# Optimization experiments

Hardware: AMD Instinct MI355X
Metric: run time of the kernel (lower is better)

Reference implementation:

```python
import jax, jax.numpy as jnp
import numpy as np

B, L, D, H, K = 1, 1024, 512, 8, 24
h = D // H
EPS = 1e-5


def setup_inputs() -> dict:
    key = jax.random.key(0)
    ks = jax.random.split(key, 8)
    s = 0.02
    return {
        "x": jax.random.normal(ks[0], (B, L, D), jnp.float32),
        "Wq": jax.random.normal(ks[1], (D, D), jnp.float32) * s,
        "bq": jnp.zeros((D,), jnp.float32),
        "Wk": jax.random.normal(ks[2], (D, D), jnp.float32) * s,
        "bk": jnp.zeros((D,), jnp.float32),
        "Wv": jax.random.normal(ks[3], (D, D), jnp.float32) * s,
        "bv": jnp.zeros((D,), jnp.float32),
        "Wo": jax.random.normal(ks[4], (D, D), jnp.float32) * s,
        "bo": jnp.zeros((D,), jnp.float32),
        "Wg": jax.random.normal(ks[5], (h * h, 1), jnp.float32) * s,
        "bg": jnp.zeros((1,), jnp.float32),
        "kv_norm_scale": jnp.ones((1, H, 1, h, h), jnp.float32),
        "qk_norm_scale": jnp.full((1, H, 1), 1.0 / np.sqrt(h), jnp.float32),
        "spectral_filters": jax.random.normal(ks[6], (L, K), jnp.float32) * 0.1,
    }


def _full_conv(filters, u, n_fft, L_out):
    # filters: [L, K], u: [B, H, L, h] -> causal FFT conv: [B, H, L, K, h]
    Ff = jnp.fft.rfft(filters, n=n_fft, axis=0)            # [F, K]
    U = jnp.fft.rfft(u, n=n_fft, axis=2)                    # [B, H, F, h]
    y = jnp.fft.irfft(U[:, :, :, None, :] * Ff[None, None, :, :, None], n=n_fft, axis=2)
    return y[:, :, :L_out]


def reference(x, Wq, bq, Wk, bk, Wv, bv, Wo, bo, Wg, bg,
              kv_norm_scale, qk_norm_scale, spectral_filters):
    Bb, Ll, Dd = x.shape
    q = (x @ Wq + bq).reshape(Bb, Ll, H, h).transpose(0, 2, 1, 3)  # [B,H,L,h]
    k = (x @ Wk + bk).reshape(Bb, Ll, H, h).transpose(0, 2, 1, 3)
    v = (x @ Wv + bv).reshape(Bb, Ll, H, h).transpose(0, 2, 1, 3)

    sim = jnp.einsum("bhld,bhld->bhl", q, k) * qk_norm_scale       # [B,H,L]

    # F.normalize(dim=-1)
    k = k / jnp.maximum(jnp.linalg.norm(k, axis=-1, keepdims=True), 1e-12)
    v = v / jnp.maximum(jnp.linalg.norm(v, axis=-1, keepdims=True), 1e-12)

    n_fft = 2 * Ll
    k = _full_conv(spectral_filters, k, n_fft, Ll)  # [B,H,L,K,h]
    v = _full_conv(spectral_filters, v, n_fft, Ll)

    Z = jnp.einsum("bhlkd,bhlke->bhlde", v, k) * kv_norm_scale     # [B,H,L,h,h]

    logits = Z.reshape(Bb, H, Ll, h * h) @ Wg + bg                  # [B,H,L,1]
    gates = jax.nn.relu(logits) ** 2 + EPS
    gates = gates[..., None]                                        # [B,H,L,1,1]
    gated_Z = gates * Z

    # Online-softmax associative scan over L for (m, s); Z/g combine is pure add -> cumsum.
    def combine(a, b):
        m_x, s_x = a
        m_y, s_y = b
        m = jnp.maximum(m_x, m_y)
        return (m, s_x * jnp.exp(m_x - m) + s_y * jnp.exp(m_y - m))

    m_scan, s_scan = jax.lax.associative_scan(combine, (sim, jnp.ones_like(sim)), axis=2)
    Z_scan = jnp.cumsum(gated_Z, axis=2)
    g_scan = jnp.cumsum(gates, axis=2)

    softmax_w = jnp.exp(sim - m_scan)[..., None, None] / (s_scan[..., None, None] + EPS)
    gated_w = Z_scan / (g_scan + EPS)
    attn = gated_w * (1.0 + jax.nn.silu(softmax_w))                 # [B,H,L,h,h]

    ctxt = jnp.einsum("bhld,bhlde->bhle", q, attn)                  # [B,H,L,h]
    ctxt = ctxt.transpose(0, 2, 1, 3).reshape(Bb, Ll, Dd)
    return ctxt @ Wo + bo
```

## Files before the change

### kernel.cpp

```cpp
#include <hip/hip_runtime.h>
#include <math.h>

#define Hh 8
#define Ll 1024
#define KF 24
#define Dm 512
#define EPSf 1e-5f
#define LK (Ll*KF)

typedef __attribute__((ext_vector_type(8))) short sh8;
typedef __attribute__((ext_vector_type(4))) short sh4;
typedef __attribute__((ext_vector_type(4))) float f32x4;

#define OFF_SIM    1572864
#define OFF_LOGITS 1581056
#define OFF_GATES  1589248
#define OFF_FACTOR 1597440
#define OFF_VCB    1605632
#define OFF_KCB    7897088
#define OFF_QPK    14188544
#define OFF_MPK    14450688
#define OFF_WOPK   14467072
#define OFF_CPK    14598144
#define OFF_CZP    26771456
#define OFF_S0     28868608
#define OFF_CPART  29392896
#define OFF_FPK_F  26771456
#define OFF_UPK_F  27607040
#define OFF_APK_F  28131328
#define OFF_BPK_F  28393472

__device__ inline unsigned short f2bf(float x){
    unsigned int u = __float_as_uint(x);
    unsigned int r = (u + 0x7fffu + ((u>>16)&1u)) >> 16;
    return (unsigned short)r;
}
__device__ inline float bf2f(unsigned short u){ return __uint_as_float(((unsigned int)u)<<16); }
__device__ inline sh8 ld8_8B(const unsigned short* p){
    union { sh8 s; sh4 h[2]; } u;
    u.h[0] = *(const sh4*)(p);
    u.h[1] = *(const sh4*)(p+4);
    return u.s;
}

__global__ __launch_bounds__(256) void pack_all_kernel(
    const float* __restrict__ x,
    const float* __restrict__ Wq, const float* __restrict__ Wk, const float* __restrict__ Wv,
    const float* __restrict__ Wo, const float* __restrict__ kvs, const float* __restrict__ Wg,
    const float* __restrict__ filt,
    unsigned short* __restrict__ Apk, unsigned short* __restrict__ Bpk,
    unsigned short* __restrict__ Wopk, unsigned short* __restrict__ Mpk,
    unsigned short* __restrict__ Fpk16, float* __restrict__ logits)
{
    int bid = blockIdx.x, tid = threadIdx.x;
    if (bid < 64){
        int mb = bid;
        for (int ks=0; ks<16; ks++){
            #pragma unroll
            for (int p=0;p<2;p++){
                int e = tid + p*256;
                int lane = e>>3, j = e&7;
                int m = mb*16 + (lane&15);
                int k = ks*32 + ((lane>>4)&3)*8 + j;
                Apk[(mb*16+ks)*512 + e] = f2bf(x[m*Dm + k]);
            }
        }
    } else if (bid < 160){
        int nb = bid - 64;
        int n0 = nb*16;
        int mm = n0>>9;
        const float* W = (mm==0)?Wq:((mm==1)?Wk:Wv);
        int coff = n0 & 511;
        for (int ks=0; ks<16; ks++){
            #pragma unroll
            for (int p=0;p<2;p++){
                int e = tid + p*256;
                int lane = e>>3, j = e&7;
                int kk = ks*32 + ((lane>>4)&3)*8 + j;
                Bpk[(nb*16+ks)*512 + e] = f2bf(W[kk*Dm + coff + (lane&15)]);
            }
        }
    } else if (bid < 192){
        int nb = bid - 160;
        int n0 = nb*16;
        for (int ks=0; ks<16; ks++){
            #pragma unroll
            for (int p=0;p<2;p++){
                int e = tid + p*256;
                int lane = e>>3, j = e&7;
                int kk = ks*32 + ((lane>>4)&3)*8 + j;
                Wopk[(nb*16+ks)*512 + e] = f2bf(Wo[kk*Dm + n0 + (lane&15)]);
            }
        }
    } else if (bid < 200){
        int hd = bid - 192;
        for (int it=0; it<16; it++){
            int idx = tid + it*256;
            int f = idx & 511, ksnb = idx >> 9;
            int nb = ksnb>>1, ks = ksnb&1;
            int lane = f>>3, j = f&7;
            int e = nb*16 + (lane&15);
            int d = ks*32 + ((lane>>4)&3)*8 + j;
            Mpk[hd*4096 + idx] = f2bf(kvs[(hd*64+e)*64 + d]*Wg[e*64+d]);
        }
    } else if (bid < 296){
        int b2 = bid - 200;
        for (int ti=0; ti<16; ti++){
            int tile = b2*16 + ti;
            int kf = tile>>6, d16 = tile&63;
            unsigned short* dst = Fpk16 + tile*1024;
            #pragma unroll
            for (int p2=0;p2<4;p2++){
                int e = tid + p2*256;
                int ks = e>>9, f = e&511;
                int lane = f>>3, j = f&7;
                int m = lane&15;
                int k = ks*32 + ((lane>>4)&3)*8 + j;
                int fidx = 16*d16 + m - k;
                float v = (fidx>=0 && fidx<Ll) ? filt[fidx*KF+kf] : 0.0f;
                dst[e] = f2bf(v);
            }
        }
    } else {
        for (int i=tid; i<Hh*Ll; i+=256) logits[i] = 0.f;
    }
}

__global__ __launch_bounds__(64) void qkvn_kernel(
    const unsigned short* __restrict__ Apk, const unsigned short* __restrict__ Bpk,
    const float* __restrict__ bq, const float* __restrict__ bk, const float* __restrict__ bv,
    const float* __restrict__ qks, float* __restrict__ simg,
    unsigned short* __restrict__ Upk, unsigned short* __restrict__ Qpk)
{
    int mb = blockIdx.x, hd = blockIdx.y;
    int lane = threadIdx.x, quad = lane>>4, lm = lane&15;
    f32x4 acc[3][4];
    #pragma unroll
    for (int mm=0;mm<3;mm++)
        #pragma unroll
        for (int nbl=0;nbl<4;nbl++) acc[mm][nbl]=(f32x4){0.f,0.f,0.f,0.f};
    for (int ks=0; ks<16; ks++){
        sh8 a = *(const sh8*)(Apk + (mb*16+ks)*512 + lane*8);
        #pragma unroll
        for (int mm=0;mm<3;mm++)
            #pragma unroll
            for (int nbl=0;nbl<4;nbl++){
                sh8 b = *(const sh8*)(Bpk + ((mm*32 + hd*4 + nbl)*16 + ks)*512 + lane*8);
                acc[mm][nbl] = __builtin_amdgcn_mfma_f32_16x16x32_bf16(a, b, acc[mm][nbl], 0,0,0);
            }
    }
    #pragma unroll
    for (int nbl=0;nbl<4;nbl++){
        float bqv = bq[hd*64 + nbl*16 + lm];
        float bkv = bk[hd*64 + nbl*16 + lm];
        float bvv = bv[hd*64 + nbl*16 + lm];
        #pragma unroll
        for (int r=0;r<4;r++){
            acc[0][nbl][r] += bqv; acc[1][nbl][r] += bkv; acc[2][nbl][r] += bvv;
        }
    }
    float simr[4], k2r[4], v2r[4];
    #pragma unroll
    for (int r=0;r<4;r++){
        float ps=0.f, pk=0.f, pv=0.f;
        #pragma unroll
        for (int nbl=0;nbl<4;nbl++){
            float qv=acc[0][nbl][r], kv=acc[1][nbl][r], vv=acc[2][nbl][r];
            ps += qv*kv; pk += kv*kv; pv += vv*vv;
        }
        #pragma unroll
        for (int off=1; off<16; off<<=1){
            ps += __shfl_xor(ps, off, 64);
            pk += __shfl_xor(pk, off, 64);
            pv += __shfl_xor(pv, off, 64);
        }
        simr[r]=ps; k2r[r]=pk; v2r[r]=pv;
    }
    float qksv = qks[hd];
    #pragma unroll
    for (int r=0;r<4;r++){
        int t = mb*16 + quad*4 + r;
        float invk = 1.f/fmaxf(sqrtf(k2r[r]), 1e-12f);
        float invv = 1.f/fmaxf(sqrtf(v2r[r]), 1e-12f);
        int ST = t>>6, ksb = (t>>5)&1, j = t&7;
        int rowf = ((t>>3)&3)*16 + lm;
        #pragma unroll
        for (int nbl=0;nbl<4;nbl++){
            int frag = ksb*2048 + nbl*512 + rowf*8 + j;
            Upk[((hd*16)+ST)*4096 + frag]     = f2bf(acc[2][nbl][r]*invv);
            Upk[(((8+hd)*16)+ST)*4096 + frag] = f2bf(acc[1][nbl][r]*invk);
            int d = nbl*16 + lm;
            int ks2 = d>>5, j2 = d&7, fl2 = ((d>>3)&3)*16 + (t&15);
            Qpk[((hd*64+mb)*2+ks2)*512 + fl2*8 + j2] = f2bf(acc[0][nbl][r]);
        }
        if (lm==0) simg[hd*Ll + t] = simr[r]*qksv;
    }
}

__device__ __forceinline__ void conv_phase(
    int T, int kf0, int hd,
    const unsigned short* __restrict__ Fpk16,
    const unsigned short* __restrict__ Uv, const unsigned short* __restrict__ Uk,
    const unsigned short* __restrict__ Mh,
    unsigned short* __restrict__ vcb, unsigned short* __restrict__ kcb,
    float* __restrict__ logits, unsigned short* lds,
    int tid, int w, int lane)
{
    int quad = lane>>4, lm = lane&15;
    f32x4 acc[3][2][4];
    #pragma unroll
    for (int kf=0;kf<3;kf++)
        #pragma unroll
        for (int tz=0;tz<2;tz++)
            #pragma unroll
            for (int nb=0;nb<4;nb++) acc[kf][tz][nb]=(f32x4){0.f,0.f,0.f,0.f};

    __syncthreads();
    {
        sh8 v0=*(const sh8*)(Uv+tid*8), v1=*(const sh8*)(Uv+(tid+256)*8);
        sh8 k0=*(const sh8*)(Uk+tid*8), k1=*(const sh8*)(Uk+(tid+256)*8);
        *(sh8*)(&lds[tid*8])=v0; *(sh8*)(&lds[(tid+256)*8])=v1;
        *(sh8*)(&lds[4096+tid*8])=k0; *(sh8*)(&lds[4096+(tid+256)*8])=k1;
    }
    for (int ST=0; ST<=T; ST++){
        sh8 nv0,nv1,nk0,nk1;
        bool more = (ST < T);
        if (more){
            const unsigned short* Uvn = Uv + (ST+1)*4096;
            const unsigned short* Ukn = Uk + (ST+1)*4096;
            nv0=*(const sh8*)(Uvn+tid*8); nv1=*(const sh8*)(Uvn+(tid+256)*8);
            nk0=*(const sh8*)(Ukn+tid*8); nk1=*(const sh8*)(Ukn+(tid+256)*8);
        }
        int d16 = 4*(T-ST) + w;
        sh8 a[3][2];
        #pragma unroll
        for (int kf=0;kf<3;kf++)
            #pragma unroll
            for (int ks=0;ks<2;ks++)
                a[kf][ks] = *(const sh8*)(Fpk16 + ((kf0+kf)*64 + d16)*1024 + ks*512 + lane*8);
        __syncthreads();
        const unsigned short* Bb = &lds[(ST&1)*8192];
        #pragma unroll
        for (int ks=0;ks<2;ks++)
            #pragma unroll
            for (int nb=0;nb<4;nb++){
                sh8 bv = *(const sh8*)(Bb + ks*2048 + nb*512 + lane*8);
                sh8 bk = *(const sh8*)(Bb + 4096 + ks*2048 + nb*512 + lane*8);
                #pragma unroll
                for (int kf=0;kf<3;kf++){
                    acc[kf][0][nb] = __builtin_amdgcn_mfma_f32_16x16x32_bf16(
                        a[kf][ks], bv, acc[kf][0][nb], 0,0,0);
                    acc[kf][1][nb] = __builtin_amdgcn_mfma_f32_16x16x32_bf16(
                        a[kf][ks], bk, acc[kf][1][nb], 0,0,0);
                }
            }
        if (more){
            unsigned short* Bn = &lds[((ST+1)&1)*8192];
            *(sh8*)(Bn+tid*8)=nv0; *(sh8*)(Bn+(tid+256)*8)=nv1;
            *(sh8*)(Bn+4096+tid*8)=nk0; *(sh8*)(Bn+4096+(tid+256)*8)=nk1;
        }
    }
    float logacc[4] = {0.f,0.f,0.f,0.f};
    #pragma unroll
    for (int kf=0;kf<3;kf++){
        __syncthreads();
        #pragma unroll
        for (int tz=0;tz<2;tz++)
            #pragma unroll
            for (int nb=0;nb<4;nb++)
                #pragma unroll
                for (int r=0;r<4;r++){
                    int tl = w*16 + quad*4 + r;
                    lds[tz*4608 + tl*72 + nb*16 + lm] = f2bf(acc[kf][tz][nb][r]);
                }
        __syncthreads();
        #pragma unroll
        for (int tz=0;tz<2;tz++){
            unsigned short* dst = tz ? kcb : vcb;
            #pragma unroll
            for (int it=0; it<2; it++){
                int idx = tid + it*256;
                int row = idx>>3, seg = idx&7;
                sh8 vv = *(const sh8*)(&lds[tz*4608 + row*72 + seg*8]);
                *(sh8*)(dst + ((hd*Ll + T*64 + row)*KF + kf0+kf)*64 + seg*8) = vv;
            }
        }
        f32x4 accp[4];
        #pragma unroll
        for (int nb=0;nb<4;nb++) accp[nb]=(f32x4){0.f,0.f,0.f,0.f};
        #pragma unroll
        for (int ks=0;ks<2;ks++){
            sh8 a2 = *(const sh8*)(&lds[4608 + (w*16+lm)*72 + ks*32 + quad*8]);
            #pragma unroll
            for (int nb=0;nb<4;nb++){
                sh8 bm = *(const sh8*)(Mh + (nb*2+ks)*512 + lane*8);
                accp[nb] = __builtin_amdgcn_mfma_f32_16x16x32_bf16(a2, bm, accp[nb], 0,0,0);
            }
        }
        #pragma unroll
        for (int r=0;r<4;r++){
            int rloc = w*16 + quad*4 + r;
            float s = 0.f;
            #pragma unroll
            for (int nb=0;nb<4;nb++)
                s += accp[nb][r]*bf2f(lds[rloc*72 + nb*16 + lm]);
            logacc[r] += s;
        }
    }
    #pragma unroll
    for (int r=0;r<4;r++){
        float s = logacc[r];
        s += __shfl_xor(s, 1, 64);
        s += __shfl_xor(s, 2, 64);
        s += __shfl_xor(s, 4, 64);
        s += __shfl_xor(s, 8, 64);
        if (lm==0)
            atomicAdd(&logits[hd*Ll + T*64 + w*16 + quad*4 + r], s);
    }
}

__global__ __launch_bounds__(256,2) void convf_kernel(
    const unsigned short* __restrict__ Fpk16, const unsigned short* __restrict__ Upk,
    const unsigned short* __restrict__ Mpk,
    unsigned short* __restrict__ vcb, unsigned short* __restrict__ kcb,
    float* __restrict__ logits)
{
    __shared__ unsigned short lds[16384];
    int p = blockIdx.x, kf0 = blockIdx.y*3, hd = blockIdx.z;
    int tid=threadIdx.x, w=tid>>6, lane=tid&63;
    const unsigned short* Uv = Upk + (hd*16)*4096;
    const unsigned short* Uk = Upk + ((8+hd)*16)*4096;
    const unsigned short* Mh = Mpk + hd*4096;
    conv_phase(15-p, kf0, hd, Fpk16, Uv, Uk, Mh, vcb, kcb, logits, lds, tid, w, lane);
    conv_phase(p,    kf0, hd, Fpk16, Uv, Uk, Mh, vcb, kcb, logits, lds, tid, w, lane);
}

__global__ __launch_bounds__(256) void scan_kernel(
    const float* __restrict__ simg, const float* __restrict__ logits,
    const float* __restrict__ bg, float* __restrict__ gates, float* __restrict__ factor)
{
    int hd=blockIdx.x, tid=threadIdx.x;
    __shared__ float sm[256], ssc[256], sg[256];
    float bgv = bg[0];
    float simv[4], m_loc[4], s_loc[4], g_loc[4];
    float m = -__builtin_inff(), s = 0.f, g = 0.f;
    for(int e=0;e<4;e++){
        int ix = hd*Ll + tid*4 + e;
        simv[e] = simg[ix];
        float lg = logits[ix] + bgv;
        float r = fmaxf(lg, 0.f);
        float gv = r*r + EPSf;
        gates[ix] = gv;
        float mn = fmaxf(m, simv[e]);
        s = s*__expf(m-mn) + __expf(simv[e]-mn);
        m = mn; g += gv;
        m_loc[e]=m; s_loc[e]=s; g_loc[e]=g;
    }
    sm[tid]=m; ssc[tid]=s; sg[tid]=g;
    __syncthreads();
    for(int off=1; off<256; off<<=1){
        float pm=0, ps=0, pg=0; bool has = (tid>=off);
        if(has){ pm=sm[tid-off]; ps=ssc[tid-off]; pg=sg[tid-off]; }
        __syncthreads();
        if(has){
            float mn=fmaxf(pm, sm[tid]);
            float sn=ps*__expf(pm-mn) + ssc[tid]*__expf(sm[tid]-mn);
            sm[tid]=mn; ssc[tid]=sn; sg[tid]=pg+sg[tid];
        }
        __syncthreads();
    }
    float pm=-__builtin_inff(), ps=0.f, pg=0.f;
    if (tid>0){ pm=sm[tid-1]; ps=ssc[tid-1]; pg=sg[tid-1]; }
    for(int e=0;e<4;e++){
        float mn=fmaxf(pm, m_loc[e]);
        float sn=ps*__expf(pm-mn) + s_loc[e]*__expf(m_loc[e]-mn);
        float gn=pg + g_loc[e];
        float sw = __expf(simv[e]-mn)/(sn+EPSf);
        float silu = sw/(1.f+__expf(-sw));
        factor[hd*Ll + tid*4 + e] = (1.f+silu)/(gn+EPSf);
    }
}

#define VTS 68
#define ASS 72
__global__ __launch_bounds__(256) void p3cz_kernel(
    const unsigned short* __restrict__ Qpk,
    const unsigned short* __restrict__ vcb, const unsigned short* __restrict__ kcb,
    const float* __restrict__ gates, float* __restrict__ cpart,
    unsigned short* __restrict__ czp)
{
    __shared__ unsigned short VT[64*VTS];
    __shared__ unsigned short KT[64*VTS];
    __shared__ unsigned short As[4][16*ASS];
    __shared__ unsigned short Vraw[64*72];
    __shared__ float gl[16];
    int tid=threadIdx.x, w=tid>>6, lane=tid&63;
    int quad=lane>>4, lm=lane&15;
    int c=blockIdx.x, qq=blockIdx.y, hd=blockIdx.z;
    int T0=c*64, tq0=T0+qq*16, RQ0=tq0*KF;
    if (tid<16) gl[tid]=gates[hd*Ll+tq0+tid];
    sh8 aq[2];
    {
        const unsigned short* qb = Qpk + ((hd*64 + (c*4+w))*2)*512;
        aq[0] = *(const sh8*)(qb + lane*8);
        aq[1] = *(const sh8*)(qb + 512 + lane*8);
    }
    f32x4 ctx[4], cz[4];
    #pragma unroll
    for (int nb=0;nb<4;nb++){ ctx[nb]=(f32x4){0,0,0,0}; cz[nb]=(f32x4){0,0,0,0}; }
    int t_g = T0 + w*16 + quad*4;
    int rp = tid>>3, e0 = (tid&7)*8, r0 = rp*2;

    sh8 pv0, pv1, pk0, pk1;
    {
        const unsigned short* vrow = vcb + (hd*LK + RQ0)*64;
        const unsigned short* krow = kcb + (hd*LK + RQ0)*64;
        pv0 = *(const sh8*)(vrow + r0*64 + e0);
        pv1 = *(const sh8*)(vrow + (r0+1)*64 + e0);
        pk0 = *(const sh8*)(krow + r0*64 + e0);
        pk1 = *(const sh8*)(krow + (r0+1)*64 + e0);
    }
    for (int sub=0; sub<6; sub++){
        int RB = RQ0 + sub*64;
        __syncthreads();
        {
            float g0 = gl[(RB + r0)/KF - tq0];
            float g1 = gl[(RB + r0 + 1)/KF - tq0];
            *(sh8*)(&Vraw[r0*72 + e0]) = pv0;
            *(sh8*)(&Vraw[(r0+1)*72 + e0]) = pv1;
            #pragma unroll
            for (int j=0;j<8;j++){
                unsigned int pv = (unsigned int)f2bf(bf2f((unsigned short)pv0[j])*g0)
                                | ((unsigned int)f2bf(bf2f((unsigned short)pv1[j])*g1)<<16);
                *(unsigned int*)(&VT[(e0+j)*VTS + r0]) = pv;
                unsigned int pk = (unsigned int)(unsigned short)pk0[j]
                                | ((unsigned int)(unsigned short)pk1[j]<<16);
                *(unsigned int*)(&KT[(e0+j)*VTS + r0]) = pk;
            }
        }
        if (sub < 5){
            const unsigned short* vrow = vcb + (hd*LK + RB + 64)*64;
            const unsigned short* krow = kcb + (hd*LK + RB + 64)*64;
            pv0 = *(const sh8*)(vrow + r0*64 + e0);
            pv1 = *(const sh8*)(vrow + (r0+1)*64 + e0);
            pk0 = *(const sh8*)(krow + r0*64 + e0);
            pk1 = *(const sh8*)(krow + (r0+1)*64 + e0);
        }
        __syncthreads();
        f32x4 S[4];
        #pragma unroll
        for (int nb=0;nb<4;nb++) S[nb]=(f32x4){0,0,0,0};
        #pragma unroll
        for (int ks=0;ks<2;ks++){
            #pragma unroll
            for (int nb=0;nb<4;nb++){
                sh8 b = *(const sh8*)(&Vraw[(nb*16+lm)*72 + ks*32 + quad*8]);
                S[nb] = __builtin_amdgcn_mfma_f32_16x16x32_bf16(aq[ks], b, S[nb], 0,0,0);
            }
        }
        #pragma unroll
        for (int nb=0;nb<4;nb++){
            int row_l = nb*16+lm;
            int tp = (RB + row_l)/KF;
            float g = gl[tp - tq0];
            #pragma unroll
            for (int r=0;r<4;r++){
                float v = (t_g + r >= tp) ? S[nb][r]*g : 0.f;
                As[w][(quad*4+r)*ASS + row_l] = f2bf(v);
            }
        }
        #pragma unroll
        for (int ks=0;ks<2;ks++){
            sh8 a2 = *(const sh8*)(&As[w][lm*ASS + ks*32 + quad*8]);
            sh8 av = ld8_8B(&VT[(w*16+lm)*VTS + ks*32 + quad*8]);
            #pragma unroll
            for (int nb=0;nb<4;nb++){
                sh8 bk = ld8_8B(&KT[(nb*16+lm)*VTS + ks*32 + quad*8]);
                ctx[nb] = __builtin_amdgcn_mfma_f32_16x16x32_bf16(a2, bk, ctx[nb], 0,0,0);
                cz[nb]  = __builtin_amdgcn_mfma_f32_16x16x32_bf16(av, bk, cz[nb], 0,0,0);
            }
        }
    }
    #pragma unroll
    for (int nb=0;nb<4;nb++){
        #pragma unroll
        for (int r=0;r<4;r++){
            cpart[((qq*8+hd)*Ll + t_g + r)*64 + nb*16+lm] = ctx[nb][r];
        }
    }
    int ob = ((hd*16+c)*4+qq)*4096;
    #pragma unroll
    for (int nb=0;nb<4;nb++){
        #pragma unroll
        for (int r=0;r<4;r++){
            czp[ob + (w*16+quad*4+r)*64 + nb*16+lm] = f2bf(cz[nb][r]);
        }
    }
}

__global__ __launch_bounds__(256) void s0_kernel(
    const unsigned short* __restrict__ czp, unsigned short* __restrict__ S0b)
{
    int idx = blockIdx.x*256 + threadIdx.x;
    int hd = blockIdx.y;
    int d = idx>>6, e = idx&63;
    int frag = (d>>5)*2048 + (e>>4)*512 + ((((d>>3)&3)*16) + (e&15))*8 + (d&7);
    float a = 0.f;
    for (int c=0;c<16;c++){
        S0b[(hd*16+c)*4096 + frag] = f2bf(a);
        int b = ((hd*16+c)*4)*4096 + idx;
        a += bf2f(czp[b]) + bf2f(czp[b+4096]) + bf2f(czp[b+2*4096]) + bf2f(czp[b+3*4096]);
    }
}

__global__ __launch_bounds__(256) void combine_kernel(
    const unsigned short* __restrict__ Qpk, const unsigned short* __restrict__ S0b,
    const float* __restrict__ cpart, const float* __restrict__ factor,
    unsigned short* __restrict__ Cpk)
{
    int c=blockIdx.x, hd=blockIdx.y;
    int tid=threadIdx.x, wid=tid>>6, lane=tid&63, quad=lane>>4, lm=lane&15;
    int mb = c*4 + wid;
    sh8 aq0 = *(const sh8*)(Qpk + ((hd*64+mb)*2)*512 + lane*8);
    sh8 aq1 = *(const sh8*)(Qpk + ((hd*64+mb)*2+1)*512 + lane*8);
    const unsigned short* sb = S0b + (hd*16+c)*4096;
    f32x4 acc[4];
    #pragma unroll
    for (int nb=0;nb<4;nb++) acc[nb]=(f32x4){0.f,0.f,0.f,0.f};
    #pragma unroll
    for (int ks=0;ks<2;ks++){
        sh8 a = ks ? aq1 : aq0;
        #pragma unroll
        for (int nb=0;nb<4;nb++){
            sh8 b = *(const sh8*)(sb + ks*2048 + nb*512 + lane*8);
            acc[nb] = __builtin_amdgcn_mfma_f32_16x16x32_bf16(a, b, acc[nb], 0,0,0);
        }
    }
    float fv[4];
    #pragma unroll
    for (int r=0;r<4;r++) fv[r] = factor[hd*Ll + mb*16 + quad*4 + r];
    #pragma unroll
    for (int nb=0;nb<4;nb++){
        int e = nb*16 + lm;
        int dim = hd*64 + e;
        int ks2 = dim>>5, koff = dim&31, qd = koff>>3, jj = koff&7;
        #pragma unroll
        for (int r=0;r<4;r++){
            int t = mb*16 + quad*4 + r;
            float v = acc[nb][r];
            #pragma unroll
            for (int q=0;q<4;q++) v += cpart[((q*8+hd)*Ll + t)*64 + e];
            v *= fv[r];
            Cpk[((t>>4)*16 + ks2)*512 + qd*128 + (t&15)*8 + jj] = f2bf(v);
        }
    }
}

__global__ __launch_bounds__(256) void outprojm_kernel(
    const unsigned short* __restrict__ Cpk, const unsigned short* __restrict__ Wopk,
    const float* __restrict__ bo, float* __restrict__ out)
{
    int mt=blockIdx.x, nt=blockIdx.y;
    int tid=threadIdx.x, wid=tid>>6, lane=tid&63;
    int mb=mt*4+wid;
    f32x4 acc[4];
    #pragma unroll
    for (int nb=0;nb<4;nb++) acc[nb]=(f32x4){0.f,0.f,0.f,0.f};
    for (int ks=0;ks<16;ks++){
        sh8 a = *(const sh8*)(Cpk + (mb*16+ks)*512 + lane*8);
        #pragma unroll
        for (int nb2=0;nb2<4;nb2++){
            sh8 b = *(const sh8*)(Wopk + ((nt*4+nb2)*16+ks)*512 + lane*8);
            acc[nb2] = __builtin_amdgcn_mfma_f32_16x16x32_bf16(a, b, acc[nb2], 0,0,0);
        }
    }
    int quad=lane>>4, col=lane&15;
    #pragma unroll
    for (int nb2=0;nb2<4;nb2++){
        int n = nt*64 + nb2*16 + col;
        float bval = bo[n];
        #pragma unroll
        for (int r=0;r<4;r++){
            out[(mb*16+quad*4+r)*Dm + n] = acc[nb2][r] + bval;
        }
    }
}

extern "C" void kernel_launch(void* const* d_in, const int* in_sizes, int n_in,
                              void* d_out, int out_size, void* d_ws, size_t ws_size,
                              hipStream_t stream)
{
    (void)in_sizes; (void)n_in; (void)out_size; (void)ws_size;
    const float* x   =(const float*)d_in[0];
    const float* Wq  =(const float*)d_in[1];
    const float* bq  =(const float*)d_in[2];
    const float* Wk  =(const float*)d_in[3];
    const float* bk  =(const float*)d_in[4];
    const float* Wv  =(const float*)d_in[5];
    const float* bv  =(const float*)d_in[6];
    const float* Wo  =(const float*)d_in[7];
    const float* bo  =(const float*)d_in[8];
    const float* Wg  =(const float*)d_in[9];
    const float* bg  =(const float*)d_in[10];
    const float* kvs =(const float*)d_in[11];
    const float* qks =(const float*)d_in[12];
    const float* filt=(const float*)d_in[13];
    float* ws = (float*)d_ws;
    float* simg  = ws+OFF_SIM;
    float* logits= ws+OFF_LOGITS;
    float* gates = ws+OFF_GATES;
    float* factor= ws+OFF_FACTOR;
    float* cpart = ws+OFF_CPART;
    unsigned short* vcb  = (unsigned short*)(ws + OFF_VCB);
    unsigned short* kcb  = (unsigned short*)(ws + OFF_KCB);
    unsigned short* Qpk  = (unsigned short*)(ws + OFF_QPK);
    unsigned short* Mpk  = (unsigned short*)(ws + OFF_MPK);
    unsigned short* Wopk = (unsigned short*)(ws + OFF_WOPK);
    unsigned short* Cpk  = (unsigned short*)(ws + OFF_CPK);
    unsigned short* czp  = (unsigned short*)(ws + OFF_CZP);
    unsigned short* S0b  = (unsigned short*)(ws + OFF_S0);
    unsigned short* Fpk16= (unsigned short*)(ws + OFF_FPK_F);
    unsigned short* Upk  = (unsigned short*)(ws + OFF_UPK_F);
    unsigned short* Apk  = (unsigned short*)(ws + OFF_APK_F);
    unsigned short* Bpk  = (unsigned short*)(ws + OFF_BPK_F);
    float* out   = (float*)d_out;

    pack_all_kernel<<<dim3(297),    256,0,stream>>>(x,Wq,Wk,Wv,Wo,kvs,Wg,filt,
                                                    Apk,Bpk,Wopk,Mpk,Fpk16,logits);
    qkvn_kernel   <<<dim3(64,8),    64, 0,stream>>>(Apk,Bpk,bq,bk,bv,qks,simg,Upk,Qpk);
    convf_kernel  <<<dim3(8,8,8),   256,0,stream>>>(Fpk16,Upk,Mpk,vcb,kcb,logits);
    scan_kernel   <<<dim3(8),       256,0,stream>>>(simg,logits,bg,gates,factor);
    p3cz_kernel   <<<dim3(16,4,8),  256,0,stream>>>(Qpk,vcb,kcb,gates,cpart,czp);
    s0_kernel     <<<dim3(16,8),    256,0,stream>>>(czp,S0b);
    combine_kernel<<<dim3(16,8),    256,0,stream>>>(Qpk,S0b,cpart,factor,Cpk);
    outprojm_kernel<<<dim3(16,8),   256,0,stream>>>(Cpk,Wopk,bo,out);
}
```

Baseline: 171.0 us.

## Fuse chunk-prefix sum into combine, atomically reduce cpart, stage filters in LDS

Removes the s0 kernel. Each combine block now computes its own exclusive prefix over earlier chunk partial sums of czp into shared memory. The four per-quarter ctx partials are now accumulated with float atomicAdd into one cpart buffer, which the pack kernel zeroes with 64 extra blocks, so combine reads one value instead of four. The filter-packing blocks also stage one filter column in LDS instead of doing strided global gathers. The trade-offs are redundant prefix work that grows with the chunk index, atomic contention, and sum order that is not deterministic.

```diff
diff --git a/kernel.cpp b/kernel.cpp
--- a/kernel.cpp
+++ b/kernel.cpp
@@ -23,7 +23,6 @@
 #define OFF_WOPK   14467072
 #define OFF_CPK    14598144
 #define OFF_CZP    26771456
-#define OFF_S0     28868608
 #define OFF_CPART  29392896
 #define OFF_FPK_F  26771456
 #define OFF_UPK_F  27607040
@@ -50,8 +49,10 @@
     const float* __restrict__ filt,
     unsigned short* __restrict__ Apk, unsigned short* __restrict__ Bpk,
     unsigned short* __restrict__ Wopk, unsigned short* __restrict__ Mpk,
-    unsigned short* __restrict__ Fpk16, float* __restrict__ logits)
-{
+    unsigned short* __restrict__ Fpk16, float* __restrict__ logits,
+    float* __restrict__ cpart)
+{
+    __shared__ float fl[1024];
     int bid = blockIdx.x, tid = threadIdx.x;
     if (bid < 64){
         int mb = bid;
@@ -105,10 +106,12 @@
         }
     } else if (bid < 296){
         int b2 = bid - 200;
+        int kf = b2>>2, g = b2&3;
+        for (int i=tid; i<1024; i+=256) fl[i] = filt[i*KF + kf];
+        __syncthreads();
         for (int ti=0; ti<16; ti++){
-            int tile = b2*16 + ti;
-            int kf = tile>>6, d16 = tile&63;
-            unsigned short* dst = Fpk16 + tile*1024;
+            int d16 = g*16 + ti;
+            unsigned short* dst = Fpk16 + (kf*64 + d16)*1024;
             #pragma unroll
             for (int p2=0;p2<4;p2++){
                 int e = tid + p2*256;
@@ -117,12 +120,16 @@
                 int m = lane&15;
                 int k = ks*32 + ((lane>>4)&3)*8 + j;
                 int fidx = 16*d16 + m - k;
-                float v = (fidx>=0 && fidx<Ll) ? filt[fidx*KF+kf] : 0.0f;
+                float v = (fidx>=0) ? fl[fidx] : 0.0f;
                 dst[e] = f2bf(v);
             }
         }
+    } else if (bid == 296){
+        for (int i=tid; i<Hh*Ll; i+=256) logits[i] = 0.f;
     } else {
-        for (int i=tid; i<Hh*Ll; i+=256) logits[i] = 0.f;
+        int zb = bid - 297;
+        int base = zb*8192;
+        for (int i=tid; i<8192; i+=256) cpart[base+i] = 0.f;
     }
 }
 
@@ -485,7 +492,7 @@
     for (int nb=0;nb<4;nb++){
         #pragma unroll
         for (int r=0;r<4;r++){
-            cpart[((qq*8+hd)*Ll + t_g + r)*64 + nb*16+lm] = ctx[nb][r];
+            atomicAdd(&cpart[(hd*Ll + t_g + r)*64 + nb*16+lm], ctx[nb][r]);
         }
     }
     int ob = ((hd*16+c)*4+qq)*4096;
@@ -498,32 +505,30 @@
     }
 }
 
-__global__ __launch_bounds__(256) void s0_kernel(
-    const unsigned short* __restrict__ czp, unsigned short* __restrict__ S0b)
-{
-    int idx = blockIdx.x*256 + threadIdx.x;
-    int hd = blockIdx.y;
-    int d = idx>>6, e = idx&63;
-    int frag = (d>>5)*2048 + (e>>4)*512 + ((((d>>3)&3)*16) + (e&15))*8 + (d&7);
-    float a = 0.f;
-    for (int c=0;c<16;c++){
-        S0b[(hd*16+c)*4096 + frag] = f2bf(a);
-        int b = ((hd*16+c)*4)*4096 + idx;
-        a += bf2f(czp[b]) + bf2f(czp[b+4096]) + bf2f(czp[b+2*4096]) + bf2f(czp[b+3*4096]);
-    }
-}
-
 __global__ __launch_bounds__(256) void combine_kernel(
-    const unsigned short* __restrict__ Qpk, const unsigned short* __restrict__ S0b,
+    const unsigned short* __restrict__ Qpk, const unsigned short* __restrict__ czp,
     const float* __restrict__ cpart, const float* __restrict__ factor,
     unsigned short* __restrict__ Cpk)
 {
+    __shared__ unsigned short sb[4096];
     int c=blockIdx.x, hd=blockIdx.y;
     int tid=threadIdx.x, wid=tid>>6, lane=tid&63, quad=lane>>4, lm=lane&15;
+    for (int it=0; it<16; it++){
+        int de = tid + it*256;
+        float a = 0.f;
+        const unsigned short* base = czp + (hd*64)*4096 + de;
+        for (int cc=0; cc<c; cc++){
+            const unsigned short* b4 = base + cc*4*4096;
+            a += bf2f(b4[0]) + bf2f(b4[4096]) + bf2f(b4[8192]) + bf2f(b4[12288]);
+        }
+        int d = de>>6, e = de&63;
+        int frag = (d>>5)*2048 + (e>>4)*512 + ((((d>>3)&3)*16)+(e&15))*8 + (d&7);
+        sb[frag] = f2bf(a);
+    }
+    __syncthreads();
     int mb = c*4 + wid;
     sh8 aq0 = *(const sh8*)(Qpk + ((hd*64+mb)*2)*512 + lane*8);
     sh8 aq1 = *(const sh8*)(Qpk + ((hd*64+mb)*2+1)*512 + lane*8);
-    const unsigned short* sb = S0b + (hd*16+c)*4096;
     f32x4 acc[4];
     #pragma unroll
     for (int nb=0;nb<4;nb++) acc[nb]=(f32x4){0.f,0.f,0.f,0.f};
@@ -547,9 +552,7 @@
         #pragma unroll
         for (int r=0;r<4;r++){
             int t = mb*16 + quad*4 + r;
-            float v = acc[nb][r];
-            #pragma unroll
-            for (int q=0;q<4;q++) v += cpart[((q*8+hd)*Ll + t)*64 + e];
+            float v = acc[nb][r] + cpart[(hd*Ll + t)*64 + e];
             v *= fv[r];
             Cpk[((t>>4)*16 + ks2)*512 + qd*128 + (t&15)*8 + jj] = f2bf(v);
         }
@@ -618,20 +621,18 @@
     unsigned short* Wopk = (unsigned short*)(ws + OFF_WOPK);
     unsigned short* Cpk  = (unsigned short*)(ws + OFF_CPK);
     unsigned short* czp  = (unsigned short*)(ws + OFF_CZP);
-    unsigned short* S0b  = (unsigned short*)(ws + OFF_S0);
     unsigned short* Fpk16= (unsigned short*)(ws + OFF_FPK_F);
     unsigned short* Upk  = (unsigned short*)(ws + OFF_UPK_F);
     unsigned short* Apk  = (unsigned short*)(ws + OFF_APK_F);
     unsigned short* Bpk  = (unsigned short*)(ws + OFF_BPK_F);
     float* out   = (float*)d_out;
 
-    pack_all_kernel<<<dim3(297),    256,0,stream>>>(x,Wq,Wk,Wv,Wo,kvs,Wg,filt,
-                                                    Apk,Bpk,Wopk,Mpk,Fpk16,logits);
+    pack_all_kernel<<<dim3(361),    256,0,stream>>>(x,Wq,Wk,Wv,Wo,kvs,Wg,filt,
+                                                    Apk,Bpk,Wopk,Mpk,Fpk16,logits,cpart);
     qkvn_kernel   <<<dim3(64,8),    64, 0,stream>>>(Apk,Bpk,bq,bk,bv,qks,simg,Upk,Qpk);
     convf_kernel  <<<dim3(8,8,8),   256,0,stream>>>(Fpk16,Upk,Mpk,vcb,kcb,logits);
     scan_kernel   <<<dim3(8),       256,0,stream>>>(simg,logits,bg,gates,factor);
     p3cz_kernel   <<<dim3(16,4,8),  256,0,stream>>>(Qpk,vcb,kcb,gates,cpart,czp);
-    s0_kernel     <<<dim3(16,8),    256,0,stream>>>(czp,S0b);
-    combine_kernel<<<dim3(16,8),    256,0,stream>>>(Qpk,S0b,cpart,factor,Cpk);
+    combine_kernel<<<dim3(16,8),    256,0,stream>>>(Qpk,czp,cpart,factor,Cpk);
     outprojm_kernel<<<dim3(16,8),   256,0,stream>>>(Cpk,Wopk,bo,out);
 }
```

Result: slower. 231.3 us (+35.3%).
